# Performance work log

Measured on AMD Instinct MI355X. Metric: run time of the kernel, lower is better.

## Reference

```python
import jax, jax.numpy as jnp
import numpy as np

# dims
B, Cin, Chid, H, W = 4, 64, 96, 64, 64
N, R, K = 16, 6, 4            # d_state, dt_rank=ceil(96/16), 4 scan directions
Dn = int(2.0 * Chid)          # d_inner = ssm_ratio * hidden_dim = 192
L = H * W


def setup_inputs():
    key = jax.random.key(0)
    ks = jax.random.split(key, 16)
    f = lambda k, shp, s=0.02: (jax.random.normal(k, shp, jnp.float32) * s)
    return dict(
        pre=jax.random.normal(ks[0], (B, Cin, H, W), jnp.float32),
        post=jax.random.normal(ks[1], (B, Cin, H, W), jnp.float32),
        prepost_w=f(ks[2], (Cin, Cin)), prepost_b=jnp.zeros((Cin,), jnp.float32),
        prepost_bn_g=jnp.ones((Cin,), jnp.float32), prepost_bn_b=jnp.zeros((Cin,), jnp.float32),
        down_w=f(ks[3], (Chid, Cin)), down_b=jnp.zeros((Chid,), jnp.float32),
        down_bn_g=jnp.ones((Chid,), jnp.float32), down_bn_b=jnp.zeros((Chid,), jnp.float32),
        up_w=f(ks[4], (Cin, Chid)), up_b=jnp.zeros((Cin,), jnp.float32),
        up_bn_g=jnp.ones((Cin,), jnp.float32), up_bn_b=jnp.zeros((Cin,), jnp.float32),
        pe_w=f(ks[5], (Chid, Chid)), pe_b=jnp.zeros((Chid,), jnp.float32),
        pe_ln_g=jnp.ones((Chid,), jnp.float32), pe_ln_b=jnp.zeros((Chid,), jnp.float32),
        in_proj_w=f(ks[6], (2 * Dn, Chid)), in_proj_b=jnp.zeros((2 * Dn,), jnp.float32),
        conv_w=f(ks[7], (Dn, 1, 3, 3), 0.1), conv_b=jnp.zeros((Dn,), jnp.float32),
        x_proj_w=f(ks[8], (K, R + 2 * N, Dn)),
        dt_w=f(ks[9], (K, Dn, R), 0.1), dt_b=f(ks[10], (K, Dn), 0.1),
        A_log=jnp.tile(jnp.log(jnp.arange(1, N + 1, dtype=jnp.float32)), (K, Dn, 1)),
        Ds=jnp.ones((K, Dn), jnp.float32),
        out_ln_g=jnp.ones((Dn,), jnp.float32), out_ln_b=jnp.zeros((Dn,), jnp.float32),
        out_proj_w=f(ks[11], (Chid, Dn)), out_proj_b=jnp.zeros((Chid,), jnp.float32),
    )


def _bn(x, g, b):  # inference BatchNorm2d (running mean=0, var=1), NCHW
    inv = g / jnp.sqrt(1.0 + 1e-5)
    return x * inv[None, :, None, None] + b[None, :, None, None]


def _conv1x1(x, w, b):  # x NCHW, w (O,C)
    return jnp.einsum('bchw,oc->bohw', x, w) + b[None, :, None, None]


def _ln(x, g, b):  # LayerNorm over last dim
    m = x.mean(-1, keepdims=True)
    v = x.var(-1, keepdims=True)
    return (x - m) / jnp.sqrt(v + 1e-5) * g + b


def _selective_scan(xs, dts, Bs, Cs, A, D, dtb):
    # xs,dts: (B,K,Dn,L); Bs,Cs: (B,K,N,L); A: (K,Dn,N); D,dtb: (K,Dn)
    delta = jax.nn.softplus(dts + dtb[None, :, :, None])

    def step(h, t):
        d_t, B_t, C_t, x_t = t  # (B,K,Dn),(B,K,N),(B,K,N),(B,K,Dn)
        h = jnp.exp(d_t[..., None] * A) * h + (d_t * x_t)[..., None] * B_t[:, :, None, :]
        return h, jnp.einsum('bkdn,bkn->bkd', h, C_t)

    mv = lambda a: jnp.moveaxis(a, -1, 0)
    h0 = jnp.zeros(xs.shape[:3] + (A.shape[-1],), xs.dtype)
    _, ys = jax.lax.scan(step, h0, (mv(delta), mv(Bs), mv(Cs), mv(xs)))
    return jnp.moveaxis(ys, 0, -1) + D[None, :, :, None] * xs


def _ss4d(x, in_proj_w, in_proj_b, conv_w, conv_b, x_proj_w, dt_w, dt_b,
          A_log, Ds, out_ln_g, out_ln_b, out_proj_w, out_proj_b):
    # x: (B,H,W,Chid) -> (B,H,W,Chid). VMamba-style 4-direction selective scan.
    xz = jnp.einsum('bhwc,oc->bhwo', x, in_proj_w) + in_proj_b
    xc, z = jnp.split(xz, 2, axis=-1)
    xc = jnp.transpose(xc, (0, 3, 1, 2))  # (B,Dn,H,W)
    xc = jax.lax.conv_general_dilated(
        xc, conv_w, (1, 1), [(1, 1), (1, 1)], feature_group_count=Dn,
        dimension_numbers=('NCHW', 'OIHW', 'NCHW')) + conv_b[None, :, None, None]
    xc = jax.nn.silu(xc)
    b, d, h, w = xc.shape
    l = h * w
    x1 = xc.reshape(b, d, l)
    x2 = jnp.transpose(xc, (0, 1, 3, 2)).reshape(b, d, l)
    xs = jnp.stack([x1, x2], 1)
    xs = jnp.concatenate([xs, jnp.flip(xs, -1)], 1)  # (B,4,Dn,L)
    x_dbl = jnp.einsum('bkdl,kcd->bkcl', xs, x_proj_w)
    dts, Bs, Cs = jnp.split(x_dbl, [R, R + N], axis=2)
    dts = jnp.einsum('bkrl,kdr->bkdl', dts, dt_w)
    A = -jnp.exp(A_log)
    ys = _selective_scan(xs, dts, Bs, Cs, A, Ds, dt_b)  # (B,4,Dn,L)
    y0, y1, y2, y3 = ys[:, 0], ys[:, 1], ys[:, 2], ys[:, 3]
    y2 = jnp.flip(y2, -1)
    y3 = jnp.flip(y3, -1)
    tb = lambda y: jnp.transpose(y.reshape(b, d, w, h), (0, 1, 3, 2)).reshape(b, d, l)
    y = y0 + y2 + tb(y1) + tb(y3)
    y = jnp.transpose(y.reshape(b, d, h, w), (0, 2, 3, 1))  # NHWC
    y = _ln(y, out_ln_g, out_ln_b)
    y = y * jax.nn.silu(z)
    return jnp.einsum('bhwd,od->bhwo', y, out_proj_w) + out_proj_b


def reference(pre, post, prepost_w, prepost_b, prepost_bn_g, prepost_bn_b,
              down_w, down_b, down_bn_g, down_bn_b, up_w, up_b, up_bn_g, up_bn_b,
              pe_w, pe_b, pe_ln_g, pe_ln_b, in_proj_w, in_proj_b, conv_w, conv_b,
              x_proj_w, dt_w, dt_b, A_log, Ds, out_ln_g, out_ln_b,
              out_proj_w, out_proj_b):
    diff = jnp.abs(post - pre)
    xres = diff
    d = jax.nn.silu(_bn(_conv1x1(diff, down_w, down_b), down_bn_g, down_bn_b))  # down
    d = _conv1x1(d, pe_w, pe_b)                                                 # patch_embed conv (k=1)
    d = _ln(jnp.transpose(d, (0, 2, 3, 1)), pe_ln_g, pe_ln_b)                   # NHWC + LN
    d = _ss4d(d, in_proj_w, in_proj_b, conv_w, conv_b, x_proj_w, dt_w, dt_b,
              A_log, Ds, out_ln_g, out_ln_b, out_proj_w, out_proj_b)
    d = jnp.transpose(d, (0, 3, 1, 2))                                          # NCHW
    d = jax.nn.silu(_bn(_conv1x1(d, up_w, up_b), up_bn_g, up_bn_b))             # up
    d = d + xres
    g1 = jax.nn.sigmoid(jax.nn.silu(_bn(_conv1x1(pre, prepost_w, prepost_b), prepost_bn_g, prepost_bn_b)))
    g2 = jax.nn.sigmoid(jax.nn.silu(_bn(_conv1x1(post, prepost_w, prepost_b), prepost_bn_g, prepost_bn_b)))
    return d * g1 * g2
```

## Files before the change

### kernel.cpp

```cpp
#include <hip/hip_runtime.h>
#include <math.h>

#define DEV static __device__ __forceinline__

constexpr int Bn = 4, CinC = 64, ChidC = 96, DnC = 192, Ll = 4096;
constexpr int Kk = 4, Rr = 6, Nn = 16;
constexpr int CH = 32, NCH = Ll / CH;

DEV float sigmoidf_(float x) { return 1.0f / (1.0f + __expf(-x)); }
DEV float siluf_(float x) { return x * sigmoidf_(x); }

DEV int pos_k(int k, int t) {
    switch (k & 3) {
        case 0: return t;
        case 1: return (t & 63) * 64 + (t >> 6);
        case 2: return Ll - 1 - t;
        default: { int s = Ll - 1 - t; return (s & 63) * 64 + (s >> 6); }
    }
}
DEV int pstride_k(int k) { return (k == 0) ? 1 : (k == 1) ? 64 : (k == 2) ? -1 : -64; }

DEV float4 ld4s(const float* p) { return *(const float4*)p; }

__global__ __launch_bounds__(256) void k1_gate_diff(
    const float* __restrict__ pre, const float* __restrict__ post,
    const float* __restrict__ w, const float* __restrict__ bias,
    const float* __restrict__ bng, const float* __restrict__ bnb,
    float* __restrict__ diff, float* __restrict__ g12)
{
    __shared__ alignas(16) float preS[64][64];
    __shared__ alignas(16) float postS[64][64];
    __shared__ alignas(16) float Ws[64][64];
    int blk = blockIdx.x;
    int tile = blk & 63, b = blk >> 6;
    int l0 = tile * 64, tid = threadIdx.x;
    for (int e = tid; e < 64 * 64; e += 256) {
        int c = e >> 6, j = e & 63;
        preS[c][j]  = pre [(size_t)(b * 64 + c) * Ll + l0 + j];
        postS[c][j] = post[(size_t)(b * 64 + c) * Ll + l0 + j];
        int o = e & 63, c2 = e >> 6;
        Ws[c2][o] = w[o * 64 + c2];
    }
    __syncthreads();
    int tx = tid & 15, ty = tid >> 4;
    float a1[4][4], a2[4][4];
#pragma unroll
    for (int i = 0; i < 4; i++)
#pragma unroll
        for (int j = 0; j < 4; j++) { a1[i][j] = 0.f; a2[i][j] = 0.f; }
    for (int c = 0; c < 64; c++) {
        float4 x1 = ld4s(&preS[c][tx * 4]);
        float4 x2 = ld4s(&postS[c][tx * 4]);
        float4 wv = ld4s(&Ws[c][ty * 4]);
        float wr[4] = {wv.x, wv.y, wv.z, wv.w};
        float x1r[4] = {x1.x, x1.y, x1.z, x1.w};
        float x2r[4] = {x2.x, x2.y, x2.z, x2.w};
#pragma unroll
        for (int i = 0; i < 4; i++)
#pragma unroll
            for (int j = 0; j < 4; j++) {
                a1[i][j] += wr[i] * x1r[j];
                a2[i][j] += wr[i] * x2r[j];
            }
    }
#pragma unroll
    for (int i = 0; i < 4; i++) {
        int o = ty * 4 + i;
        float inv = bng[o] * rsqrtf(1.0f + 1e-5f);
        float bo = bias[o], bb = bnb[o];
        float4 gv, dv;
        float* gp = (float*)&gv; float* dp = (float*)&dv;
#pragma unroll
        for (int j = 0; j < 4; j++) {
            float v1 = (a1[i][j] + bo) * inv + bb;
            float v2 = (a2[i][j] + bo) * inv + bb;
            gp[j] = sigmoidf_(siluf_(v1)) * sigmoidf_(siluf_(v2));
            dp[j] = fabsf(postS[o][tx * 4 + j] - preS[o][tx * 4 + j]);
        }
        size_t idx = (size_t)(b * 64 + o) * Ll + l0 + tx * 4;
        *(float4*)&g12[idx] = gv;
        *(float4*)&diff[idx] = dv;
    }
}

__global__ __launch_bounds__(384) void kA1_downpe(
    const float* __restrict__ diff,
    const float* __restrict__ down_w, const float* __restrict__ down_b,
    const float* __restrict__ down_bn_g, const float* __restrict__ down_bn_b,
    const float* __restrict__ pe_w, const float* __restrict__ pe_b,
    const float* __restrict__ pe_ln_g, const float* __restrict__ pe_ln_b,
    float* __restrict__ xln)
{
    __shared__ alignas(16) float sX[64][64];
    __shared__ alignas(16) float Ws[96 * 96];
    __shared__ alignas(16) float sH[96][64];
    __shared__ alignas(16) float mrs[2][64];
    int blk = blockIdx.x;
    int tile = blk & 63, b = blk >> 6;
    int l0 = tile * 64, tid = threadIdx.x;
    int tx = tid & 15, ty = tid >> 4;
    for (int e = tid; e < 64 * 64; e += 384) {
        int c = e >> 6, j = e & 63;
        sX[c][j] = diff[(size_t)(b * 64 + c) * Ll + l0 + j];
// ... 85 lines not shown
#pragma unroll
    for (int i = 0; i < 4; i++) {
        int o = ty * 4 + i;
        float gg = pe_ln_g[o], bb = pe_ln_b[o];
        float4 ov; float* op = (float*)&ov;
#pragma unroll
        for (int j = 0; j < 4; j++) op[j] = (a2[i][j] - mj[j]) * rj[j] * gg + bb;
        *(float4*)&xln[(size_t)(b * 96 + o) * Ll + l0 + tx * 4] = ov;
    }
}

__global__ __launch_bounds__(256) void kA2_inproj(
    const float* __restrict__ xln, const float* __restrict__ w, const float* __restrict__ bias,
    float* __restrict__ xc_cm, float* __restrict__ z_pm)
{
    __shared__ alignas(16) float Xs[96][64];
    __shared__ alignas(16) float Ws[96][128];
    int blk = blockIdx.x;
    int ot = blk % 3; int rest = blk / 3;
    int tile = rest & 63, b = rest >> 6;
    int l0 = tile * 64, o0 = ot * 128, tid = threadIdx.x;
    for (int e = tid; e < 96 * 64; e += 256) {
        int c = e >> 6, j = e & 63;
        Xs[c][j] = xln[(size_t)(b * 96 + c) * Ll + l0 + j];
    }
    for (int e = tid; e < 96 * 128; e += 256) {
        int o = e & 127, c = e >> 7;
        Ws[c][o] = w[(o0 + o) * 96 + c];
    }
    __syncthreads();
    int tx = tid & 15, ty = tid >> 4;
    float acc[8][4];
#pragma unroll
    for (int i = 0; i < 8; i++)
#pragma unroll
        for (int j = 0; j < 4; j++) acc[i][j] = 0.f;
    for (int c = 0; c < 96; c++) {
        float4 xv = ld4s(&Xs[c][tx * 4]);
        float4 w0 = ld4s(&Ws[c][ty * 8]);
        float4 w1 = ld4s(&Ws[c][ty * 8 + 4]);
        float wr[8] = {w0.x, w0.y, w0.z, w0.w, w1.x, w1.y, w1.z, w1.w};
        float xr[4] = {xv.x, xv.y, xv.z, xv.w};
#pragma unroll
        for (int i = 0; i < 8; i++)
#pragma unroll
            for (int j = 0; j < 4; j++) acc[i][j] += wr[i] * xr[j];
    }
#pragma unroll
    for (int i = 0; i < 8; i++) {
        int og = o0 + ty * 8 + i;
        float bo = bias[og];
#pragma unroll
        for (int j = 0; j < 4; j++) acc[i][j] += bo;
    }
#pragma unroll
    for (int i = 0; i < 8; i++) {
        int og = o0 + ty * 8 + i;
        if (og < 192) {
            float4 ov; float* op = (float*)&ov;
#pragma unroll
            for (int j = 0; j < 4; j++) op[j] = acc[i][j];
            *(float4*)&xc_cm[(size_t)(b * DnC + og) * Ll + l0 + tx * 4] = ov;
        }
    }
    if (o0 + ty * 8 + 7 >= 192) {
#pragma unroll
        for (int i0 = 0; i0 < 8; i0 += 4) {
            int og = o0 + ty * 8 + i0;
            if (og < 192) continue;
            int zo = og - 192;
#pragma unroll
            for (int j = 0; j < 4; j++) {
                float4 ov; float* op = (float*)&ov;
#pragma unroll
                for (int i = 0; i < 4; i++) op[i] = acc[i0 + i][j];
                *(float4*)&z_pm[(size_t)(b * Ll + l0 + tx * 4 + j) * DnC + zo] = ov;
            }
        }
    }
}

__global__ __launch_bounds__(256) void kB_dwconv_t(
    const float* __restrict__ xc_cm, const float* __restrict__ conv_w,
    const float* __restrict__ conv_b, float* __restrict__ xs_pm)
{
    __shared__ float tr[64][97];
    int blk = blockIdx.x;
    int dh = blk & 1, h = (blk >> 1) & 63, b = blk >> 7;
    int d0 = dh * 96;
    int tid = threadIdx.x;
#pragma unroll 4
    for (int it = 0; it < 24; it++) {
        int o = it * 256 + tid;
        int d = o >> 6, w = o & 63, dd = d0 + d;
        const float* base = xc_cm + (size_t)(b * DnC + dd) * Ll;
        float acc = conv_b[dd];
#pragma unroll
        for (int kh = 0; kh < 3; kh++) {
            int hh = h + kh - 1;
            if ((unsigned)hh >= 64u) continue;
#pragma unroll
            for (int kw = 0; kw < 3; kw++) {
                int ww = w + kw - 1;
                if ((unsigned)ww >= 64u) continue;
                acc += base[hh * 64 + ww] * conv_w[dd * 9 + kh * 3 + kw];
            }
        }
        tr[w][d] = siluf_(acc);
    }
    __syncthreads();
    for (int e = tid; e < 64 * 96; e += 256) {
        int w = e / 96, d = e % 96;
        xs_pm[(size_t)(b * Ll + h * 64 + w) * DnC + d0 + d] = tr[w][d];
    }
}

__global__ __launch_bounds__(192) void k8_xdbl(
    const float* __restrict__ xs_pm, const float* __restrict__ xpw,
    float* __restrict__ xdbl)
{
    __shared__ alignas(16) float Xs[64][68];
    __shared__ alignas(16) float Ws[64][48];
    int blk = blockIdx.x;
    int tile = blk & 63, k = (blk >> 6) & 3, b = blk >> 8;
    int t0 = tile * 64, tid = threadIdx.x;
    int tx = tid & 15, ty = tid >> 4;
    for (int e = tid; e < 64 * 48; e += 192) ((float*)Ws)[e] = 0.f;
    float acc[4][4];
#pragma unroll
    for (int i = 0; i < 4; i++)
#pragma unroll
        for (int j = 0; j < 4; j++) acc[i][j] = 0.f;
    for (int cc = 0; cc < 192; cc += 64) {
        __syncthreads();
        for (int e = tid; e < 64 * 64; e += 192) {
            int d = e & 63, j = e >> 6;
            int p = pos_k(k, t0 + j);
            Xs[d][j] = xs_pm[(size_t)(b * Ll + p) * DnC + cc + d];
        }
        for (int e = tid; e < 38 * 64; e += 192) {
            int d = e & 63, c = e >> 6;
            Ws[d][c] = xpw[(size_t)(k * 38 + c) * DnC + cc + d];
        }
        __syncthreads();
        for (int d = 0; d < 64; d++) {
            float4 xv = ld4s(&Xs[d][tx * 4]);
            float4 wv = ld4s(&Ws[d][ty * 4]);
            float wr[4] = {wv.x, wv.y, wv.z, wv.w};
            float xr[4] = {xv.x, xv.y, xv.z, xv.w};
#pragma unroll
            for (int i = 0; i < 4; i++)
#pragma unroll
                for (int j = 0; j < 4; j++) acc[i][j] += wr[i] * xr[j];
        }
    }
#pragma unroll
    for (int i = 0; i < 4; i++) {
        int o = ty * 4 + i;
        if (o < 38) {
            float4 ov; float* op = (float*)&ov;
#pragma unroll
            for (int j = 0; j < 4; j++) op[j] = acc[i][j];
            *(float4*)&xdbl[((size_t)(b * Kk + k) * 38 + o) * Ll + t0 + tx * 4] = ov;
        }
    }
}

__global__ __launch_bounds__(384) void k10_scanA(
    const float* __restrict__ xdbl, const float* __restrict__ xs_pm,
    const float* __restrict__ dt_w, const float* __restrict__ dt_b,
    float* __restrict__ Sbuf, float* __restrict__ Ubuf)
{
    __shared__ alignas(16) float dts_s[2][CH][8];
    __shared__ alignas(16) float bs_s[2][CH][20];
    int blk = blockIdx.x;
    int cp = blk & 63, k = (blk >> 6) & 3, b = blk >> 8;
    int tid = threadIdx.x;
    int sub = (tid >= 192) ? 1 : 0;
    int d = tid - sub * 192;
    int ch = cp * 2 + sub;
    int t0 = ch * CH;
    const float* xd = xdbl + (size_t)(b * Kk + k) * 38 * Ll;
    for (int e = d; e < CH * Rr; e += 192) {
        int c = e >> 5, j = e & 31;
        dts_s[sub][j][c] = xd[(size_t)c * Ll + t0 + j];
    }
    for (int e = d; e < CH * Nn; e += 192) {
        int c = e >> 5, j = e & 31;
        bs_s[sub][j][c] = xd[(size_t)(Rr + c) * Ll + t0 + j];
    }
    float dtw[Rr];
#pragma unroll
    for (int r = 0; r < Rr; r++) dtw[r] = dt_w[(size_t)(k * DnC + d) * Rr + r];
    float dtb = dt_b[k * DnC + d];
    int pbase = pos_k(k, t0), pstr = pstride_k(k);
    size_t xbase = (size_t)b * Ll * DnC + d;
    float xn = xs_pm[xbase + (size_t)pbase * DnC];
    __syncthreads();
    float h[Nn];
#pragma unroll
    for (int n = 0; n < Nn; n++) h[n] = 0.f;
    float S = 0.f;
    int p = pbase;
    for (int j = 0; j < CH; j++) {
        float x = xn;
        p += pstr;
        if (j < CH - 1) xn = xs_pm[xbase + (size_t)p * DnC];
        float4 dv0 = *(const float4*)&dts_s[sub][j][0];
        float4 dv1 = *(const float4*)&dts_s[sub][j][4];
        float dr = dtb + dv0.x * dtw[0] + dv0.y * dtw[1] + dv0.z * dtw[2]
                       + dv0.w * dtw[3] + dv1.x * dtw[4] + dv1.y * dtw[5];
        float4 b0 = *(const float4*)&bs_s[sub][j][0];
        float4 b1 = *(const float4*)&bs_s[sub][j][4];
        float4 b2 = *(const float4*)&bs_s[sub][j][8];
        float4 b3 = *(const float4*)&bs_s[sub][j][12];
        float bsr[16] = {b0.x,b0.y,b0.z,b0.w, b1.x,b1.y,b1.z,b1.w,
                         b2.x,b2.y,b2.z,b2.w, b3.x,b3.y,b3.z,b3.w};
        float er = __expf(dr);
        float e1 = __fdividef(1.0f, 1.0f + er);
        float delta = (dr > 15.f) ? dr : __logf(1.0f + er);
        S += delta;
        float dx = delta * x;
        float en = 1.f;
#pragma unroll
        for (int n = 0; n < Nn; n++) {
            en *= e1;
            h[n] = en * h[n] + dx * bsr[n];
        }
    }
    int bk = b * Kk + k;
    Sbuf[((size_t)bk * NCH + ch) * DnC + d] = S;
    size_t ubase = (((size_t)bk * NCH + ch) * DnC + d) * Nn;
    float4* ub = (float4*)&Ubuf[ubase];
#pragma unroll
    for (int q = 0; q < 4; q++) {
        float4 hv; float* hp = (float*)&hv;
#pragma unroll
        for (int i = 0; i < 4; i++) hp[i] = h[q * 4 + i];
        ub[q] = hv;
    }
}

__global__ __launch_bounds__(256) void k11_prefix(
    const float* __restrict__ Sbuf, const float* __restrict__ A_log,
    float* __restrict__ Ubuf)
{
    int gid = blockIdx.x * 256 + threadIdx.x;
    int bk = gid / (DnC * Nn);
    int dn = gid % (DnC * Nn);
    int d = dn >> 4, n = dn & 15;
    int k = bk & 3;
    float an = -__expf(A_log[(size_t)(k * DnC + d) * Nn + n]);
    size_t sbase = (size_t)bk * NCH * DnC + d;
    size_t ubase = (size_t)bk * NCH * (DnC * Nn) + dn;
    float hv = 0.f;
    for (int c0 = 0; c0 < NCH; c0 += 8) {
        float S8[8], u8[8];
#pragma unroll
        for (int t = 0; t < 8; t++) {
            S8[t] = Sbuf[sbase + (size_t)(c0 + t) * DnC];
            u8[t] = Ubuf[ubase + (size_t)(c0 + t) * (DnC * Nn)];
        }
#pragma unroll
        for (int t = 0; t < 8; t++) {
            Ubuf[ubase + (size_t)(c0 + t) * (DnC * Nn)] = hv;
            hv = __expf(an * S8[t]) * hv + u8[t];
        }
    }
}

__global__ __launch_bounds__(384) void k12_scanC(
    const float* __restrict__ xdbl, const float* __restrict__ xs_pm,
    const float* __restrict__ dt_w, const float* __restrict__ dt_b,
    const float* __restrict__ Ubuf, float* __restrict__ ycomb)
{
    __shared__ alignas(16) float dts_s[2][CH][8];
    __shared__ alignas(16) float bs_s[2][CH][20];
    __shared__ alignas(16) float cs_s[2][CH][20];
    int blk = blockIdx.x;
    int cp = blk & 63, k = (blk >> 6) & 3, b = blk >> 8;
    int tid = threadIdx.x;
    int sub = (tid >= 192) ? 1 : 0;
    int d = tid - sub * 192;
    int ch = cp * 2 + sub;
    int t0 = ch * CH;
    const float* xd = xdbl + (size_t)(b * Kk + k) * 38 * Ll;
    for (int e = d; e < CH * Rr; e += 192) {
        int c = e >> 5, j = e & 31;
        dts_s[sub][j][c] = xd[(size_t)c * Ll + t0 + j];
    }
    for (int e = d; e < CH * Nn; e += 192) {
        int c = e >> 5, j = e & 31;
        bs_s[sub][j][c] = xd[(size_t)(Rr + c) * Ll + t0 + j];
        cs_s[sub][j][c] = xd[(size_t)(Rr + Nn + c) * Ll + t0 + j];
    }
    float dtw[Rr];
#pragma unroll
    for (int r = 0; r < Rr; r++) dtw[r] = dt_w[(size_t)(k * DnC + d) * Rr + r];
    float dtb = dt_b[k * DnC + d];
    int bk = b * Kk + k;
    int pbase = pos_k(k, t0), pstr = pstride_k(k);
    size_t xbase = (size_t)b * Ll * DnC + d;
    float h[Nn];
    size_t ubase = (((size_t)bk * NCH + ch) * DnC + d) * Nn;
    const float4* ub = (const float4*)&Ubuf[ubase];
#pragma unroll
    for (int q = 0; q < 4; q++) {
        float4 hv = ub[q];
        h[q * 4 + 0] = hv.x; h[q * 4 + 1] = hv.y; h[q * 4 + 2] = hv.z; h[q * 4 + 3] = hv.w;
    }
    float xn = xs_pm[xbase + (size_t)pbase * DnC];
    __syncthreads();
    int p = pbase;
    for (int j = 0; j < CH; j++) {
        float x = xn;
        int pcur = p;
        p += pstr;
        if (j < CH - 1) xn = xs_pm[xbase + (size_t)p * DnC];
        float4 dv0 = *(const float4*)&dts_s[sub][j][0];
        float4 dv1 = *(const float4*)&dts_s[sub][j][4];
        float dr = dtb + dv0.x * dtw[0] + dv0.y * dtw[1] + dv0.z * dtw[2]
                       + dv0.w * dtw[3] + dv1.x * dtw[4] + dv1.y * dtw[5];
        float4 b0 = *(const float4*)&bs_s[sub][j][0];
        float4 b1 = *(const float4*)&bs_s[sub][j][4];
        float4 b2 = *(const float4*)&bs_s[sub][j][8];
        float4 b3 = *(const float4*)&bs_s[sub][j][12];
        float bsr[16] = {b0.x,b0.y,b0.z,b0.w, b1.x,b1.y,b1.z,b1.w,
                         b2.x,b2.y,b2.z,b2.w, b3.x,b3.y,b3.z,b3.w};
        float4 c0 = *(const float4*)&cs_s[sub][j][0];
        float4 c1 = *(const float4*)&cs_s[sub][j][4];
        float4 c2 = *(const float4*)&cs_s[sub][j][8];
        float4 c3 = *(const float4*)&cs_s[sub][j][12];
        float csr[16] = {c0.x,c0.y,c0.z,c0.w, c1.x,c1.y,c1.z,c1.w,
                         c2.x,c2.y,c2.z,c2.w, c3.x,c3.y,c3.z,c3.w};
        float er = __expf(dr);
        float e1 = __fdividef(1.0f, 1.0f + er);
        float delta = (dr > 15.f) ? dr : __logf(1.0f + er);
        float dx = delta * x;
        float y = 0.f;
        float en = 1.f;
#pragma unroll
        for (int n = 0; n < Nn; n++) {
            en *= e1;
            h[n] = en * h[n] + dx * bsr[n];
            y += h[n] * csr[n];
        }
        atomicAdd(&ycomb[(size_t)(b * Ll + pcur) * DnC + d], y);
    }
}

__global__ __launch_bounds__(256) void k13_gate_ln(
    float* __restrict__ ycomb, const float* __restrict__ z_pm,
    const float* __restrict__ xs_pm, const float* __restrict__ Dsp,
    const float* __restrict__ g, const float* __restrict__ be)
{
    int wid = threadIdx.x >> 6, lane = threadIdx.x & 63;
    int posi = blockIdx.x * 4 + wid;
    size_t base = (size_t)posi * DnC;
    float vs[3];
#pragma unroll
    for (int jj = 0; jj < 3; jj++) {
        int dd = lane + 64 * jj;
        float sd = Dsp[dd] + Dsp[DnC + dd] + Dsp[2 * DnC + dd] + Dsp[3 * DnC + dd];
        vs[jj] = ycomb[base + dd] + sd * xs_pm[base + dd];
    }
    float s = vs[0] + vs[1] + vs[2];
    float s2 = vs[0] * vs[0] + vs[1] * vs[1] + vs[2] * vs[2];
#pragma unroll
    for (int off = 32; off >= 1; off >>= 1) {
        s  += __shfl_xor(s, off);
        s2 += __shfl_xor(s2, off);
    }
    float m = s / 192.f;
    float var = s2 / 192.f - m * m;
    float rstd = rsqrtf(var + 1e-5f);
#pragma unroll
    for (int jj = 0; jj < 3; jj++) {
        int dd = lane + 64 * jj;
        float yln = (vs[jj] - m) * rstd * g[dd] + be[dd];
        float zv = z_pm[base + dd];
        ycomb[base + dd] = yln * siluf_(zv);
    }
}

__global__ __launch_bounds__(384) void kC_outproj(
    const float* __restrict__ y_pm, const float* __restrict__ opw, const float* __restrict__ opb,
    float* __restrict__ u_cm)
{
    __shared__ alignas(16) float Xs[64][68];
    __shared__ alignas(16) float Ws[64][96];
    int blk = blockIdx.x;
    int tile = blk & 63, b = blk >> 6;
    int l0 = tile * 64, tid = threadIdx.x;
    int tx = tid & 15, ty = tid >> 4;
    float acc[4][4];
#pragma unroll
    for (int i = 0; i < 4; i++)
#pragma unroll
        for (int j = 0; j < 4; j++) acc[i][j] = 0.f;
    for (int cc = 0; cc < 192; cc += 64) {
        __syncthreads();
        for (int e = tid; e < 64 * 64; e += 384) {
            int c = e & 63, p = e >> 6;
            Xs[c][p] = y_pm[(size_t)(b * Ll + l0 + p) * DnC + cc + c];
        }
        for (int e = tid; e < 64 * 96; e += 384) {
            int o = e % 96, c = e / 96;
            Ws[c][o] = opw[(size_t)o * DnC + cc + c];
        }
        __syncthreads();
        for (int c = 0; c < 64; c++) {
            float4 xv = ld4s(&Xs[c][tx * 4]);
            float4 wv = ld4s(&Ws[c][ty * 4]);
            float wr[4] = {wv.x, wv.y, wv.z, wv.w};
            float xr[4] = {xv.x, xv.y, xv.z, xv.w};
#pragma unroll
            for (int i = 0; i < 4; i++)
#pragma unroll
                for (int j = 0; j < 4; j++) acc[i][j] += wr[i] * xr[j];
        }
    }
#pragma unroll
    for (int i = 0; i < 4; i++) {
        int o = ty * 4 + i;
        float bo = opb[o];
        float4 ov; float* op = (float*)&ov;
#pragma unroll
        for (int j = 0; j < 4; j++) op[j] = acc[i][j] + bo;
        *(float4*)&u_cm[(size_t)(b * 96 + o) * Ll + l0 + tx * 4] = ov;
    }
}

__global__ __launch_bounds__(256) void kD_up_final(
    const float* __restrict__ u_cm, const float* __restrict__ upw, const float* __restrict__ upb,
    const float* __restrict__ ubng, const float* __restrict__ ubnb,
    const float* __restrict__ diff, const float* __restrict__ g12,
    float* __restrict__ outp)
{
    __shared__ alignas(16) float Xs[96][64];
    __shared__ alignas(16) float Ws[96][64];
    int blk = blockIdx.x;
    int tile = blk & 63, b = blk >> 6;
    int l0 = tile * 64, tid = threadIdx.x;
    for (int e = tid; e < 96 * 64; e += 256) {
        int c = e >> 6, j = e & 63;
        Xs[c][j] = u_cm[(size_t)(b * 96 + c) * Ll + l0 + j];
        int o = e & 63, c2 = e >> 6;
        Ws[c2][o] = upw[o * 96 + c2];
    }
    __syncthreads();
    int tx = tid & 15, ty = tid >> 4;
    float acc[4][4];
#pragma unroll
    for (int i = 0; i < 4; i++)
#pragma unroll
        for (int j = 0; j < 4; j++) acc[i][j] = 0.f;
    for (int c = 0; c < 96; c++) {
        float4 xv = ld4s(&Xs[c][tx * 4]);
        float4 wv = ld4s(&Ws[c][ty * 4]);
        float wr[4] = {wv.x, wv.y, wv.z, wv.w};
        float xr[4] = {xv.x, xv.y, xv.z, xv.w};
#pragma unroll
        for (int i = 0; i < 4; i++)
#pragma unroll
            for (int j = 0; j < 4; j++) acc[i][j] += wr[i] * xr[j];
    }
#pragma unroll
    for (int i = 0; i < 4; i++) {
        int o = ty * 4 + i;
        float inv = ubng[o] * rsqrtf(1.0f + 1e-5f);
        float bo = upb[o], bb = ubnb[o];
        size_t idx = (size_t)(b * 64 + o) * Ll + l0 + tx * 4;
        float4 dv = ld4s(&diff[idx]);
        float4 gv = ld4s(&g12[idx]);
        float dr[4] = {dv.x, dv.y, dv.z, dv.w};
        float gr[4] = {gv.x, gv.y, gv.z, gv.w};
        float4 ov; float* op = (float*)&ov;
#pragma unroll
        for (int j = 0; j < 4; j++) {
            float v = siluf_((acc[i][j] + bo) * inv + bb);
            op[j] = (v + dr[j]) * gr[j];
        }
        *(float4*)&outp[idx] = ov;
    }
}

extern "C" void kernel_launch(void* const* d_in, const int* in_sizes, int n_in,
                              void* d_out, int out_size, void* d_ws, size_t ws_size,
                              hipStream_t stream)
{
    const float* pre          = (const float*)d_in[0];
    const float* post         = (const float*)d_in[1];
    const float* prepost_w    = (const float*)d_in[2];
    const float* prepost_b    = (const float*)d_in[3];
    const float* prepost_bn_g = (const float*)d_in[4];
    const float* prepost_bn_b = (const float*)d_in[5];
    const float* down_w       = (const float*)d_in[6];
    const float* down_b       = (const float*)d_in[7];
    const float* down_bn_g    = (const float*)d_in[8];
    const float* down_bn_b    = (const float*)d_in[9];
    const float* up_w         = (const float*)d_in[10];
    const float* up_b         = (const float*)d_in[11];
    const float* up_bn_g      = (const float*)d_in[12];
    const float* up_bn_b      = (const float*)d_in[13];
    const float* pe_w         = (const float*)d_in[14];
    const float* pe_b         = (const float*)d_in[15];
    const float* pe_ln_g      = (const float*)d_in[16];
    const float* pe_ln_b      = (const float*)d_in[17];
    const float* in_proj_w    = (const float*)d_in[18];
    const float* in_proj_b    = (const float*)d_in[19];
    const float* conv_w       = (const float*)d_in[20];
    const float* conv_b       = (const float*)d_in[21];
    const float* x_proj_w     = (const float*)d_in[22];
    const float* dt_w         = (const float*)d_in[23];
    const float* dt_b         = (const float*)d_in[24];
    const float* A_log        = (const float*)d_in[25];
    const float* Ds           = (const float*)d_in[26];
    const float* out_ln_g     = (const float*)d_in[27];
    const float* out_ln_b     = (const float*)d_in[28];
    const float* out_proj_w   = (const float*)d_in[29];
    const float* out_proj_b   = (const float*)d_in[30];

    float* ws     = (float*)d_ws;
    float* diff   = ws;
    float* g12    = diff + 1048576;
    float* xcz    = g12 + 1048576;
    float* z_pm   = xcz + 3145728;
    float* xs_pm  = z_pm + 3145728;
    float* xdbl   = xs_pm + 3145728;
    float* Sbuf   = xdbl + 2490368;
    float* Ubuf   = Sbuf + 393216;
    float* xln    = Ubuf;
    float* u_cm   = Ubuf;

    k1_gate_diff<<<256, 256, 0, stream>>>(pre, post, prepost_w, prepost_b,
                                          prepost_bn_g, prepost_bn_b, diff, g12);
    kA1_downpe<<<256, 384, 0, stream>>>(diff, down_w, down_b, down_bn_g, down_bn_b,
                                        pe_w, pe_b, pe_ln_g, pe_ln_b, xln);
    kA2_inproj<<<768, 256, 0, stream>>>(xln, in_proj_w, in_proj_b, xcz, z_pm);
    kB_dwconv_t<<<512, 256, 0, stream>>>(xcz, conv_w, conv_b, xs_pm);
    k8_xdbl<<<1024, 192, 0, stream>>>(xs_pm, x_proj_w, xdbl);
    hipMemsetAsync(xcz, 0, (size_t)3145728 * sizeof(float), stream);
    k10_scanA<<<1024, 384, 0, stream>>>(xdbl, xs_pm, dt_w, dt_b, Sbuf, Ubuf);
    k11_prefix<<<192, 256, 0, stream>>>(Sbuf, A_log, Ubuf);
    k12_scanC<<<1024, 384, 0, stream>>>(xdbl, xs_pm, dt_w, dt_b, Ubuf, xcz);
    k13_gate_ln<<<4096, 256, 0, stream>>>(xcz, z_pm, xs_pm, Ds, out_ln_g, out_ln_b);
    kC_outproj<<<256, 384, 0, stream>>>(xcz, out_proj_w, out_proj_b, u_cm);
    kD_up_final<<<256, 256, 0, stream>>>(u_cm, up_w, up_b, up_bn_g, up_bn_b,
                                         diff, g12, (float*)d_out);
}
```

Baseline: 407.0 us.

## Pair opposite scan directions per block and remove atomic y accumulation

```diff
diff --git a/kernel.cpp b/kernel.cpp
--- a/kernel.cpp
+++ b/kernel.cpp
@@ -9,16 +9,6 @@
 
 DEV float sigmoidf_(float x) { return 1.0f / (1.0f + __expf(-x)); }
 DEV float siluf_(float x) { return x * sigmoidf_(x); }
-
-DEV int pos_k(int k, int t) {
-    switch (k & 3) {
-        case 0: return t;
-        case 1: return (t & 63) * 64 + (t >> 6);
-        case 2: return Ll - 1 - t;
-        default: { int s = Ll - 1 - t; return (s & 63) * 64 + (s >> 6); }
-    }
-}
-DEV int pstride_k(int k) { return (k == 0) ? 1 : (k == 1) ? 64 : (k == 2) ? -1 : -64; }
 
 DEV float4 ld4s(const float* p) { return *(const float4*)p; }
 
@@ -270,7 +260,8 @@
 
 __global__ __launch_bounds__(256) void kB_dwconv_t(
     const float* __restrict__ xc_cm, const float* __restrict__ conv_w,
-    const float* __restrict__ conv_b, float* __restrict__ xs_pm)
+    const float* __restrict__ conv_b, float* __restrict__ xs_pm,
+    float* __restrict__ xs_cm)
 {
     __shared__ float tr[64][97];
     int blk = blockIdx.x;
@@ -294,7 +285,9 @@
                 acc += base[hh * 64 + ww] * conv_w[dd * 9 + kh * 3 + kw];
             }
         }
-        tr[w][d] = siluf_(acc);
+        float v = siluf_(acc);
+        tr[w][d] = v;
+        xs_cm[(size_t)(b * DnC + dd) * Ll + h * 64 + w] = v;
     }
     __syncthreads();
     for (int e = tid; e < 64 * 96; e += 256) {
@@ -303,9 +296,43 @@
     }
 }
 
+__global__ __launch_bounds__(256) void kT_transp(
+    const float* __restrict__ xs_cm, const float* __restrict__ xpw,
+    float* __restrict__ xs_cmT, float* __restrict__ xpwT)
+{
+    int blk = blockIdx.x, tid = threadIdx.x;
+    if (blk < 768) {
+        __shared__ float T[64][65];
+        int b = blk / 192, d = blk % 192;
+        const float* src = xs_cm + (size_t)(b * DnC + d) * Ll;
+        float* dst = xs_cmT + (size_t)(b * DnC + d) * Ll;
+        for (int e = tid; e < 4096; e += 256) {
+            int h = e >> 6, w = e & 63;
+            T[h][w] = src[e];
+        }
+        __syncthreads();
+        for (int e = tid; e < 4096; e += 256) {
+            int w = e >> 6, h = e & 63;
+            dst[e] = T[h][w];
+        }
+    } else {
+        int base = (blk - 768) * 1024 + tid * 4;
+        if (base < 4 * 192 * 48) {
+            int c = base % 48;
+            int d = (base / 48) % 192;
+            int k = base / (48 * 192);
+            float4 v; float* vp = (float*)&v;
+#pragma unroll
+            for (int i = 0; i < 4; i++)
+                vp[i] = (c + i < 38) ? xpw[(size_t)(k * 38 + c + i) * DnC + d] : 0.f;
+            *(float4*)&xpwT[base] = v;
+        }
+    }
+}
+
 __global__ __launch_bounds__(192) void k8_xdbl(
-    const float* __restrict__ xs_pm, const float* __restrict__ xpw,
-    float* __restrict__ xdbl)
+    const float* __restrict__ xs_cm, const float* __restrict__ xs_cmT,
+    const float* __restrict__ xpwT, float* __restrict__ xdbl)
 {
     __shared__ alignas(16) float Xs[64][68];
     __shared__ alignas(16) float Ws[64][48];
@@ -313,7 +340,8 @@
     int tile = blk & 63, k = (blk >> 6) & 3, b = blk >> 8;
     int t0 = tile * 64, tid = threadIdx.x;
     int tx = tid & 15, ty = tid >> 4;
-    for (int e = tid; e < 64 * 48; e += 192) ((float*)Ws)[e] = 0.f;
+    const float* src = (k & 1) ? xs_cmT : xs_cm;
+    bool rev = (k >= 2);
     float acc[4][4];
 #pragma unroll
     for (int i = 0; i < 4; i++)
@@ -321,19 +349,27 @@
         for (int j = 0; j < 4; j++) acc[i][j] = 0.f;
     for (int cc = 0; cc < 192; cc += 64) {
         __syncthreads();
-        for (int e = tid; e < 64 * 64; e += 192) {
-            int d = e & 63, j = e >> 6;
-            int p = pos_k(k, t0 + j);
-            Xs[d][j] = xs_pm[(size_t)(b * Ll + p) * DnC + cc + d];
-        }
-        for (int e = tid; e < 38 * 64; e += 192) {
-            int d = e & 63, c = e >> 6;
-            Ws[d][c] = xpw[(size_t)(k * 38 + c) * DnC + cc + d];
+        for (int e = tid; e < 1024; e += 192) {
+            int j4 = e & 15, dl = e >> 4;
+            const float* row = src + (size_t)(b * DnC + cc + dl) * Ll;
+            if (!rev) {
+                float4 v = *(const float4*)&row[t0 + 4 * j4];
+                *(float4*)&Xs[dl][4 * j4] = v;
+            } else {
+                float4 v = *(const float4*)&row[Ll - 4 - t0 - 4 * j4];
+                float4 r; r.x = v.w; r.y = v.z; r.z = v.y; r.w = v.x;
+                *(float4*)&Xs[dl][4 * j4] = r;
+            }
+        }
+        for (int e = tid; e < 768; e += 192) {
+            int c4 = e % 12, dl = e / 12;
+            float4 v = *(const float4*)&xpwT[((size_t)(k * DnC) + cc + dl) * 48 + 4 * c4];
+            *(float4*)&Ws[dl][4 * c4] = v;
         }
         __syncthreads();
-        for (int d = 0; d < 64; d++) {
-            float4 xv = ld4s(&Xs[d][tx * 4]);
-            float4 wv = ld4s(&Ws[d][ty * 4]);
+        for (int dl = 0; dl < 64; dl++) {
+            float4 xv = ld4s(&Xs[dl][tx * 4]);
+            float4 wv = ld4s(&Ws[dl][ty * 4]);
             float wr[4] = {wv.x, wv.y, wv.z, wv.w};
             float xr[4] = {xv.x, xv.y, xv.z, xv.w};
 #pragma unroll
@@ -354,7 +390,7 @@
     }
 }
 
-__global__ __launch_bounds__(384) void k10_scanA(
+__global__ __launch_bounds__(192) void k10_scanA(
     const float* __restrict__ xdbl, const float* __restrict__ xs_pm,
     const float* __restrict__ dt_w, const float* __restrict__ dt_b,
     float* __restrict__ Sbuf, float* __restrict__ Ubuf)
@@ -362,70 +398,119 @@
     __shared__ alignas(16) float dts_s[2][CH][8];
     __shared__ alignas(16) float bs_s[2][CH][20];
     int blk = blockIdx.x;
-    int cp = blk & 63, k = (blk >> 6) & 3, b = blk >> 8;
-    int tid = threadIdx.x;
-    int sub = (tid >= 192) ? 1 : 0;
-    int d = tid - sub * 192;
-    int ch = cp * 2 + sub;
-    int t0 = ch * CH;
-    const float* xd = xdbl + (size_t)(b * Kk + k) * 38 * Ll;
-    for (int e = d; e < CH * Rr; e += 192) {
-        int c = e >> 5, j = e & 31;
-        dts_s[sub][j][c] = xd[(size_t)c * Ll + t0 + j];
-    }
-    for (int e = d; e < CH * Nn; e += 192) {
-        int c = e >> 5, j = e & 31;
-        bs_s[sub][j][c] = xd[(size_t)(Rr + c) * Ll + t0 + j];
-    }
-    float dtw[Rr];
-#pragma unroll
-    for (int r = 0; r < Rr; r++) dtw[r] = dt_w[(size_t)(k * DnC + d) * Rr + r];
-    float dtb = dt_b[k * DnC + d];
-    int pbase = pos_k(k, t0), pstr = pstride_k(k);
+    int ch = blk & 127, pair = (blk >> 7) & 1, b = blk >> 8;
+    int ka = pair, kb = pair + 2;
+    int t0a = ch * CH, t0b = Ll - CH - t0a;
+    int d = threadIdx.x;
+    {
+        const float* xda = xdbl + (size_t)(b * Kk + ka) * 38 * Ll;
+        const float* xdb = xdbl + (size_t)(b * Kk + kb) * 38 * Ll;
+        for (int e = d; e < CH * Rr; e += 192) {
+            int c = e >> 5, j = e & 31;
+            dts_s[0][j][c] = xda[(size_t)c * Ll + t0a + j];
+            dts_s[1][j][c] = xdb[(size_t)c * Ll + t0b + j];
+        }
+        for (int e = d; e < CH * Nn; e += 192) {
+            int c = e >> 5, j = e & 31;
+            bs_s[0][j][c] = xda[(size_t)(Rr + c) * Ll + t0a + j];
+            bs_s[1][j][c] = xdb[(size_t)(Rr + c) * Ll + t0b + j];
+        }
+    }
+    float dtwa[Rr], dtwb[Rr];
+#pragma unroll
+    for (int r = 0; r < Rr; r++) {
+        dtwa[r] = dt_w[(size_t)(ka * DnC + d) * Rr + r];
+        dtwb[r] = dt_w[(size_t)(kb * DnC + d) * Rr + r];
+    }
+    float dtba = dt_b[ka * DnC + d], dtbb = dt_b[kb * DnC + d];
+    int Pb = (pair == 0) ? t0a : ((t0a & 63) * 64 + (t0a >> 6));
+    int Pstr = (pair == 0) ? 1 : 64;
     size_t xbase = (size_t)b * Ll * DnC + d;
-    float xn = xs_pm[xbase + (size_t)pbase * DnC];
-    __syncthreads();
-    float h[Nn];
-#pragma unroll
-    for (int n = 0; n < Nn; n++) h[n] = 0.f;
-    float S = 0.f;
-    int p = pbase;
-    for (int j = 0; j < CH; j++) {
-        float x = xn;
-        p += pstr;
-        if (j < CH - 1) xn = xs_pm[xbase + (size_t)p * DnC];
-        float4 dv0 = *(const float4*)&dts_s[sub][j][0];
-        float4 dv1 = *(const float4*)&dts_s[sub][j][4];
-        float dr = dtb + dv0.x * dtw[0] + dv0.y * dtw[1] + dv0.z * dtw[2]
-                       + dv0.w * dtw[3] + dv1.x * dtw[4] + dv1.y * dtw[5];
-        float4 b0 = *(const float4*)&bs_s[sub][j][0];
-        float4 b1 = *(const float4*)&bs_s[sub][j][4];
-        float4 b2 = *(const float4*)&bs_s[sub][j][8];
-        float4 b3 = *(const float4*)&bs_s[sub][j][12];
-        float bsr[16] = {b0.x,b0.y,b0.z,b0.w, b1.x,b1.y,b1.z,b1.w,
-                         b2.x,b2.y,b2.z,b2.w, b3.x,b3.y,b3.z,b3.w};
-        float er = __expf(dr);
-        float e1 = __fdividef(1.0f, 1.0f + er);
-        float delta = (dr > 15.f) ? dr : __logf(1.0f + er);
-        S += delta;
-        float dx = delta * x;
-        float en = 1.f;
-#pragma unroll
-        for (int n = 0; n < Nn; n++) {
-            en *= e1;
-            h[n] = en * h[n] + dx * bsr[n];
-        }
-    }
-    int bk = b * Kk + k;
-    Sbuf[((size_t)bk * NCH + ch) * DnC + d] = S;
-    size_t ubase = (((size_t)bk * NCH + ch) * DnC + d) * Nn;
-    float4* ub = (float4*)&Ubuf[ubase];
-#pragma unroll
-    for (int q = 0; q < 4; q++) {
-        float4 hv; float* hp = (float*)&hv;
-#pragma unroll
-        for (int i = 0; i < 4; i++) hp[i] = h[q * 4 + i];
-        ub[q] = hv;
+    __syncthreads();
+    {
+        float h[Nn];
+#pragma unroll
+        for (int n = 0; n < Nn; n++) h[n] = 0.f;
+        float S = 0.f;
+        float xn = xs_pm[xbase + (size_t)Pb * DnC];
+        for (int j = 0; j < CH; j++) {
+            float x = xn;
+            if (j < CH - 1) xn = xs_pm[xbase + (size_t)(Pb + (j + 1) * Pstr) * DnC];
+            float4 dv0 = *(const float4*)&dts_s[0][j][0];
+            float4 dv1 = *(const float4*)&dts_s[0][j][4];
+            float dr = dtba + dv0.x * dtwa[0] + dv0.y * dtwa[1] + dv0.z * dtwa[2]
+                            + dv0.w * dtwa[3] + dv1.x * dtwa[4] + dv1.y * dtwa[5];
+            float4 b0 = *(const float4*)&bs_s[0][j][0];
+            float4 b1 = *(const float4*)&bs_s[0][j][4];
+            float4 b2 = *(const float4*)&bs_s[0][j][8];
+            float4 b3 = *(const float4*)&bs_s[0][j][12];
+            float bsr[16] = {b0.x,b0.y,b0.z,b0.w, b1.x,b1.y,b1.z,b1.w,
+                             b2.x,b2.y,b2.z,b2.w, b3.x,b3.y,b3.z,b3.w};
+            float er = __expf(dr);
+            float e1 = __fdividef(1.0f, 1.0f + er);
+            float delta = (dr > 15.f) ? dr : __logf(1.0f + er);
+            S += delta;
+            float dx = delta * x;
+            float en = 1.f;
+#pragma unroll
+            for (int n = 0; n < Nn; n++) {
+                en *= e1;
+                h[n] = en * h[n] + dx * bsr[n];
+            }
+        }
+        int bk = b * Kk + ka;
+        Sbuf[((size_t)bk * NCH + ch) * DnC + d] = S;
+        float4* ub = (float4*)&Ubuf[(((size_t)bk * NCH + ch) * DnC + d) * Nn];
+#pragma unroll
+        for (int q = 0; q < 4; q++) {
+            float4 hv; float* hp = (float*)&hv;
+#pragma unroll
+            for (int i = 0; i < 4; i++) hp[i] = h[q * 4 + i];
+            ub[q] = hv;
+        }
+    }
+    {
+        float h[Nn];
+#pragma unroll
+        for (int n = 0; n < Nn; n++) h[n] = 0.f;
+        float S = 0.f;
+        float xn = xs_pm[xbase + (size_t)(Pb + (CH - 1) * Pstr) * DnC];
+        for (int j = 0; j < CH; j++) {
+            float x = xn;
+            if (j < CH - 1) xn = xs_pm[xbase + (size_t)(Pb + (CH - 2 - j) * Pstr) * DnC];
+            float4 dv0 = *(const float4*)&dts_s[1][j][0];
+            float4 dv1 = *(const float4*)&dts_s[1][j][4];
+            float dr = dtbb + dv0.x * dtwb[0] + dv0.y * dtwb[1] + dv0.z * dtwb[2]
+                            + dv0.w * dtwb[3] + dv1.x * dtwb[4] + dv1.y * dtwb[5];
+            float4 b0 = *(const float4*)&bs_s[1][j][0];
+            float4 b1 = *(const float4*)&bs_s[1][j][4];
+            float4 b2 = *(const float4*)&bs_s[1][j][8];
+            float4 b3 = *(const float4*)&bs_s[1][j][12];
+            float bsr[16] = {b0.x,b0.y,b0.z,b0.w, b1.x,b1.y,b1.z,b1.w,
+                             b2.x,b2.y,b2.z,b2.w, b3.x,b3.y,b3.z,b3.w};
+            float er = __expf(dr);
+            float e1 = __fdividef(1.0f, 1.0f + er);
+            float delta = (dr > 15.f) ? dr : __logf(1.0f + er);
+            S += delta;
+            float dx = delta * x;
+            float en = 1.f;
+#pragma unroll
+            for (int n = 0; n < Nn; n++) {
+                en *= e1;
+                h[n] = en * h[n] + dx * bsr[n];
+            }
+        }
+        int bk = b * Kk + kb;
+        int chb = NCH - 1 - ch;
+        Sbuf[((size_t)bk * NCH + chb) * DnC + d] = S;
+        float4* ub = (float4*)&Ubuf[(((size_t)bk * NCH + chb) * DnC + d) * Nn];
+#pragma unroll
+        for (int q = 0; q < 4; q++) {
+            float4 hv; float* hp = (float*)&hv;
+#pragma unroll
+            for (int i = 0; i < 4; i++) hp[i] = h[q * 4 + i];
+            ub[q] = hv;
+        }
     }
 }
 
@@ -457,90 +542,143 @@
     }
 }
 
-__global__ __launch_bounds__(384) void k12_scanC(
+__global__ __launch_bounds__(192) void k12_scanC(
     const float* __restrict__ xdbl, const float* __restrict__ xs_pm,
     const float* __restrict__ dt_w, const float* __restrict__ dt_b,
-    const float* __restrict__ Ubuf, float* __restrict__ ycomb)
+    const float* __restrict__ Ubuf, float* __restrict__ y02,
+    float* __restrict__ y13)
 {
     __shared__ alignas(16) float dts_s[2][CH][8];
     __shared__ alignas(16) float bs_s[2][CH][20];
     __shared__ alignas(16) float cs_s[2][CH][20];
     int blk = blockIdx.x;
-    int cp = blk & 63, k = (blk >> 6) & 3, b = blk >> 8;
-    int tid = threadIdx.x;
-    int sub = (tid >= 192) ? 1 : 0;
-    int d = tid - sub * 192;
-    int ch = cp * 2 + sub;
-    int t0 = ch * CH;
-    const float* xd = xdbl + (size_t)(b * Kk + k) * 38 * Ll;
-    for (int e = d; e < CH * Rr; e += 192) {
-        int c = e >> 5, j = e & 31;
-        dts_s[sub][j][c] = xd[(size_t)c * Ll + t0 + j];
-    }
-    for (int e = d; e < CH * Nn; e += 192) {
-        int c = e >> 5, j = e & 31;
-        bs_s[sub][j][c] = xd[(size_t)(Rr + c) * Ll + t0 + j];
-        cs_s[sub][j][c] = xd[(size_t)(Rr + Nn + c) * Ll + t0 + j];
-    }
-    float dtw[Rr];
-#pragma unroll
-    for (int r = 0; r < Rr; r++) dtw[r] = dt_w[(size_t)(k * DnC + d) * Rr + r];
-    float dtb = dt_b[k * DnC + d];
-    int bk = b * Kk + k;
-    int pbase = pos_k(k, t0), pstr = pstride_k(k);
+    int ch = blk & 127, pair = (blk >> 7) & 1, b = blk >> 8;
+    int ka = pair, kb = pair + 2;
+    int t0a = ch * CH, t0b = Ll - CH - t0a;
+    int d = threadIdx.x;
+    {
+        const float* xda = xdbl + (size_t)(b * Kk + ka) * 38 * Ll;
+        const float* xdb = xdbl + (size_t)(b * Kk + kb) * 38 * Ll;
+        for (int e = d; e < CH * Rr; e += 192) {
+            int c = e >> 5, j = e & 31;
+            dts_s[0][j][c] = xda[(size_t)c * Ll + t0a + j];
+            dts_s[1][j][c] = xdb[(size_t)c * Ll + t0b + j];
+        }
+        for (int e = d; e < CH * Nn; e += 192) {
+            int c = e >> 5, j = e & 31;
+            bs_s[0][j][c] = xda[(size_t)(Rr + c) * Ll + t0a + j];
+            bs_s[1][j][c] = xdb[(size_t)(Rr + c) * Ll + t0b + j];
+            cs_s[0][j][c] = xda[(size_t)(Rr + Nn + c) * Ll + t0a + j];
+            cs_s[1][j][c] = xdb[(size_t)(Rr + Nn + c) * Ll + t0b + j];
+        }
+    }
+    float dtwa[Rr], dtwb[Rr];
+#pragma unroll
+    for (int r = 0; r < Rr; r++) {
+        dtwa[r] = dt_w[(size_t)(ka * DnC + d) * Rr + r];
+        dtwb[r] = dt_w[(size_t)(kb * DnC + d) * Rr + r];
+    }
+    float dtba = dt_b[ka * DnC + d], dtbb = dt_b[kb * DnC + d];
+    int Pb = (pair == 0) ? t0a : ((t0a & 63) * 64 + (t0a >> 6));
+    int Pstr = (pair == 0) ? 1 : 64;
     size_t xbase = (size_t)b * Ll * DnC + d;
-    float h[Nn];
-    size_t ubase = (((size_t)bk * NCH + ch) * DnC + d) * Nn;
-    const float4* ub = (const float4*)&Ubuf[ubase];
-#pragma unroll
-    for (int q = 0; q < 4; q++) {
-        float4 hv = ub[q];
-        h[q * 4 + 0] = hv.x; h[q * 4 + 1] = hv.y; h[q * 4 + 2] = hv.z; h[q * 4 + 3] = hv.w;
-    }
-    float xn = xs_pm[xbase + (size_t)pbase * DnC];
-    __syncthreads();
-    int p = pbase;
-    for (int j = 0; j < CH; j++) {
-        float x = xn;
-        int pcur = p;
-        p += pstr;
-        if (j < CH - 1) xn = xs_pm[xbase + (size_t)p * DnC];
-        float4 dv0 = *(const float4*)&dts_s[sub][j][0];
-        float4 dv1 = *(const float4*)&dts_s[sub][j][4];
-        float dr = dtb + dv0.x * dtw[0] + dv0.y * dtw[1] + dv0.z * dtw[2]
-                       + dv0.w * dtw[3] + dv1.x * dtw[4] + dv1.y * dtw[5];
-        float4 b0 = *(const float4*)&bs_s[sub][j][0];
-        float4 b1 = *(const float4*)&bs_s[sub][j][4];
-        float4 b2 = *(const float4*)&bs_s[sub][j][8];
-        float4 b3 = *(const float4*)&bs_s[sub][j][12];
-        float bsr[16] = {b0.x,b0.y,b0.z,b0.w, b1.x,b1.y,b1.z,b1.w,
-                         b2.x,b2.y,b2.z,b2.w, b3.x,b3.y,b3.z,b3.w};
-        float4 c0 = *(const float4*)&cs_s[sub][j][0];
-        float4 c1 = *(const float4*)&cs_s[sub][j][4];
-        float4 c2 = *(const float4*)&cs_s[sub][j][8];
-        float4 c3 = *(const float4*)&cs_s[sub][j][12];
-        float csr[16] = {c0.x,c0.y,c0.z,c0.w, c1.x,c1.y,c1.z,c1.w,
-                         c2.x,c2.y,c2.z,c2.w, c3.x,c3.y,c3.z,c3.w};
-        float er = __expf(dr);
-        float e1 = __fdividef(1.0f, 1.0f + er);
-        float delta = (dr > 15.f) ? dr : __logf(1.0f + er);
-        float dx = delta * x;
-        float y = 0.f;
-        float en = 1.f;
-#pragma unroll
-        for (int n = 0; n < Nn; n++) {
-            en *= e1;
-            h[n] = en * h[n] + dx * bsr[n];
-            y += h[n] * csr[n];
-        }
-        atomicAdd(&ycomb[(size_t)(b * Ll + pcur) * DnC + d], y);
+    float* ybuf = pair ? y13 : y02;
+    __syncthreads();
+    {
+        float h[Nn];
+        const float4* ub = (const float4*)&Ubuf[(((size_t)(b * Kk + ka) * NCH + ch) * DnC + d) * Nn];
+#pragma unroll
+        for (int q = 0; q < 4; q++) {
+            float4 hv = ub[q];
+            h[q*4+0]=hv.x; h[q*4+1]=hv.y; h[q*4+2]=hv.z; h[q*4+3]=hv.w;
+        }
+        float xn = xs_pm[xbase + (size_t)Pb * DnC];
+        for (int j = 0; j < CH; j++) {
+            float x = xn;
+            if (j < CH - 1) xn = xs_pm[xbase + (size_t)(Pb + (j + 1) * Pstr) * DnC];
+            float4 dv0 = *(const float4*)&dts_s[0][j][0];
+            float4 dv1 = *(const float4*)&dts_s[0][j][4];
+            float dr = dtba + dv0.x * dtwa[0] + dv0.y * dtwa[1] + dv0.z * dtwa[2]
+                            + dv0.w * dtwa[3] + dv1.x * dtwa[4] + dv1.y * dtwa[5];
+            float4 b0 = *(const float4*)&bs_s[0][j][0];
+            float4 b1 = *(const float4*)&bs_s[0][j][4];
+            float4 b2 = *(const float4*)&bs_s[0][j][8];
+            float4 b3 = *(const float4*)&bs_s[0][j][12];
+            float bsr[16] = {b0.x,b0.y,b0.z,b0.w, b1.x,b1.y,b1.z,b1.w,
+                             b2.x,b2.y,b2.z,b2.w, b3.x,b3.y,b3.z,b3.w};
+            float4 c0 = *(const float4*)&cs_s[0][j][0];
+            float4 c1 = *(const float4*)&cs_s[0][j][4];
+            float4 c2 = *(const float4*)&cs_s[0][j][8];
+            float4 c3 = *(const float4*)&cs_s[0][j][12];
+            float csr[16] = {c0.x,c0.y,c0.z,c0.w, c1.x,c1.y,c1.z,c1.w,
+                             c2.x,c2.y,c2.z,c2.w, c3.x,c3.y,c3.z,c3.w};
+            float er = __expf(dr);
+            float e1 = __fdividef(1.0f, 1.0f + er);
+            float delta = (dr > 15.f) ? dr : __logf(1.0f + er);
+            float dx = delta * x;
+            float y = 0.f;
+            float en = 1.f;
+#pragma unroll
+            for (int n = 0; n < Nn; n++) {
+                en *= e1;
+                h[n] = en * h[n] + dx * bsr[n];
+                y += h[n] * csr[n];
+            }
+            ybuf[(size_t)(b * Ll + Pb + j * Pstr) * DnC + d] = y;
+        }
+    }
+    {
+        float h[Nn];
+        int chb = NCH - 1 - ch;
+        const float4* ub = (const float4*)&Ubuf[(((size_t)(b * Kk + kb) * NCH + chb) * DnC + d) * Nn];
+#pragma unroll
+        for (int q = 0; q < 4; q++) {
+            float4 hv = ub[q];
+            h[q*4+0]=hv.x; h[q*4+1]=hv.y; h[q*4+2]=hv.z; h[q*4+3]=hv.w;
+        }
+        float xn = xs_pm[xbase + (size_t)(Pb + (CH - 1) * Pstr) * DnC];
+        for (int j = 0; j < CH; j++) {
+            float x = xn;
+            if (j < CH - 1) xn = xs_pm[xbase + (size_t)(Pb + (CH - 2 - j) * Pstr) * DnC];
+            float4 dv0 = *(const float4*)&dts_s[1][j][0];
+            float4 dv1 = *(const float4*)&dts_s[1][j][4];
+            float dr = dtbb + dv0.x * dtwb[0] + dv0.y * dtwb[1] + dv0.z * dtwb[2]
+                            + dv0.w * dtwb[3] + dv1.x * dtwb[4] + dv1.y * dtwb[5];
+            float4 b0 = *(const float4*)&bs_s[1][j][0];
+            float4 b1 = *(const float4*)&bs_s[1][j][4];
+            float4 b2 = *(const float4*)&bs_s[1][j][8];
+            float4 b3 = *(const float4*)&bs_s[1][j][12];
+            float bsr[16] = {b0.x,b0.y,b0.z,b0.w, b1.x,b1.y,b1.z,b1.w,
+                             b2.x,b2.y,b2.z,b2.w, b3.x,b3.y,b3.z,b3.w};
+            float4 c0 = *(const float4*)&cs_s[1][j][0];
+            float4 c1 = *(const float4*)&cs_s[1][j][4];
+            float4 c2 = *(const float4*)&cs_s[1][j][8];
+            float4 c3 = *(const float4*)&cs_s[1][j][12];
+            float csr[16] = {c0.x,c0.y,c0.z,c0.w, c1.x,c1.y,c1.z,c1.w,
+                             c2.x,c2.y,c2.z,c2.w, c3.x,c3.y,c3.z,c3.w};
+            float er = __expf(dr);
+            float e1 = __fdividef(1.0f, 1.0f + er);
+            float delta = (dr > 15.f) ? dr : __logf(1.0f + er);
+            float dx = delta * x;
+            float y = 0.f;
+            float en = 1.f;
+#pragma unroll
+            for (int n = 0; n < Nn; n++) {
+                en *= e1;
+                h[n] = en * h[n] + dx * bsr[n];
+                y += h[n] * csr[n];
+            }
+            float* yp = &ybuf[(size_t)(b * Ll + Pb + (CH - 1 - j) * Pstr) * DnC + d];
+            *yp += y;
+        }
     }
 }
 
 __global__ __launch_bounds__(256) void k13_gate_ln(
-    float* __restrict__ ycomb, const float* __restrict__ z_pm,
-    const float* __restrict__ xs_pm, const float* __restrict__ Dsp,
-    const float* __restrict__ g, const float* __restrict__ be)
+    float* __restrict__ y02, const float* __restrict__ y13,
+    const float* __restrict__ z_pm, const float* __restrict__ xs_pm,
+    const float* __restrict__ Dsp, const float* __restrict__ g,
+    const float* __restrict__ be)
 {
     int wid = threadIdx.x >> 6, lane = threadIdx.x & 63;
     int posi = blockIdx.x * 4 + wid;
@@ -550,7 +688,7 @@
     for (int jj = 0; jj < 3; jj++) {
         int dd = lane + 64 * jj;
         float sd = Dsp[dd] + Dsp[DnC + dd] + Dsp[2 * DnC + dd] + Dsp[3 * DnC + dd];
-        vs[jj] = ycomb[base + dd] + sd * xs_pm[base + dd];
+        vs[jj] = y02[base + dd] + y13[base + dd] + sd * xs_pm[base + dd];
     }
     float s = vs[0] + vs[1] + vs[2];
     float s2 = vs[0] * vs[0] + vs[1] * vs[1] + vs[2] * vs[2];
@@ -567,7 +705,7 @@
         int dd = lane + 64 * jj;
         float yln = (vs[jj] - m) * rstd * g[dd] + be[dd];
         float zv = z_pm[base + dd];
-        ycomb[base + dd] = yln * siluf_(zv);
+        y02[base + dd] = yln * siluf_(zv);
     }
 }
 
@@ -712,28 +850,32 @@
     float* ws     = (float*)d_ws;
     float* diff   = ws;
     float* g12    = diff + 1048576;
-    float* xcz    = g12 + 1048576;
-    float* z_pm   = xcz + 3145728;
+    float* slotA  = g12 + 1048576;
+    float* z_pm   = slotA + 3145728;
     float* xs_pm  = z_pm + 3145728;
-    float* xdbl   = xs_pm + 3145728;
+    float* slotB  = xs_pm + 3145728;
+    float* xdbl   = slotB + 3145728;
     float* Sbuf   = xdbl + 2490368;
-    float* Ubuf   = Sbuf + 393216;
+    float* xpwT   = Sbuf + 393216;
+    float* Ubuf   = xpwT + 36864;
     float* xln    = Ubuf;
-    float* u_cm   = Ubuf;
+    float* xs_cmT = Ubuf;
+    float* u_cm   = Ubuf + 3145728;
 
     k1_gate_diff<<<256, 256, 0, stream>>>(pre, post, prepost_w, prepost_b,
                                           prepost_bn_g, prepost_bn_b, diff, g12);
     kA1_downpe<<<256, 384, 0, stream>>>(diff, down_w, down_b, down_bn_g, down_bn_b,
                                         pe_w, pe_b, pe_ln_g, pe_ln_b, xln);
-    kA2_inproj<<<768, 256, 0, stream>>>(xln, in_proj_w, in_proj_b, xcz, z_pm);
-    kB_dwconv_t<<<512, 256, 0, stream>>>(xcz, conv_w, conv_b, xs_pm);
-    k8_xdbl<<<1024, 192, 0, stream>>>(xs_pm, x_proj_w, xdbl);
-    hipMemsetAsync(xcz, 0, (size_t)3145728 * sizeof(float), stream);
-    k10_scanA<<<1024, 384, 0, stream>>>(xdbl, xs_pm, dt_w, dt_b, Sbuf, Ubuf);
+    kA2_inproj<<<768, 256, 0, stream>>>(xln, in_proj_w, in_proj_b, slotA, z_pm);
+    kB_dwconv_t<<<512, 256, 0, stream>>>(slotA, conv_w, conv_b, xs_pm, slotB);
+    kT_transp<<<804, 256, 0, stream>>>(slotB, x_proj_w, xs_cmT, xpwT);
+    k8_xdbl<<<1024, 192, 0, stream>>>(slotB, xs_cmT, xpwT, xdbl);
+    k10_scanA<<<1024, 192, 0, stream>>>(xdbl, xs_pm, dt_w, dt_b, Sbuf, Ubuf);
     k11_prefix<<<192, 256, 0, stream>>>(Sbuf, A_log, Ubuf);
-    k12_scanC<<<1024, 384, 0, stream>>>(xdbl, xs_pm, dt_w, dt_b, Ubuf, xcz);
-    k13_gate_ln<<<4096, 256, 0, stream>>>(xcz, z_pm, xs_pm, Ds, out_ln_g, out_ln_b);
-    kC_outproj<<<256, 384, 0, stream>>>(xcz, out_proj_w, out_proj_b, u_cm);
+    k12_scanC<<<1024, 192, 0, stream>>>(xdbl, xs_pm, dt_w, dt_b, Ubuf, slotA, slotB);
+    k13_gate_ln<<<4096, 256, 0, stream>>>(slotA, slotB, z_pm, xs_pm, Ds,
+                                          out_ln_g, out_ln_b);
+    kC_outproj<<<256, 384, 0, stream>>>(slotA, out_proj_w, out_proj_b, u_cm);
     kD_up_final<<<256, 256, 0, stream>>>(u_cm, up_w, up_b, up_bn_g, up_bn_b,
                                          diff, g12, (float*)d_out);
 }
```

New measurement: 397.1 us. -2.4%, faster.
